# Kernel tuning notes

Hardware: AMD Instinct MI355X
Metric: run time of the kernel (lower is better)

Reference implementation:

```python
import jax, jax.numpy as jnp
import numpy as np

N = 50000; E = 800000; IN_DIM = 128; HID = 128; OUT = 128; K_TARGET = 5000


def setup_inputs() -> dict:
    key = jax.random.key(0)
    ks = jax.random.split(key, 7)
    x = jax.random.normal(ks[0], (N, IN_DIM), jnp.float32)
    edge_index = jax.random.randint(ks[1], (2, E), 0, N, dtype=jnp.int32)
    W1 = jax.random.normal(ks[2], (IN_DIM, HID), jnp.float32) / np.float32(np.sqrt(IN_DIM))
    b1 = jnp.zeros((HID,), jnp.float32)
    W2 = jax.random.normal(ks[3], (HID, OUT), jnp.float32) / np.float32(np.sqrt(HID))
    b2 = jnp.zeros((OUT,), jnp.float32)
    w_score = jax.random.normal(ks[4], (HID,), jnp.float32) / np.float32(np.sqrt(HID))
    W_skip = jax.random.normal(ks[5], (HID, OUT), jnp.float32) / np.float32(np.sqrt(HID))
    b_skip = jnp.zeros((OUT,), jnp.float32)
    return dict(x=x, edge_index=edge_index, W1=W1, b1=b1, W2=W2, b2=b2,
                w_score=w_score, W_skip=W_skip, b_skip=b_skip)


def _gcn(h_in, row, col, W, b, nseg, edge_w=None):
    # PyG GCNConv with add_self_loops=True, normalize=True:
    # deg[i] = sum of incoming edge weights at col + 1 (self loop, weight 1)
    h = h_in @ W
    w = edge_w if edge_w is not None else jnp.ones(row.shape, h.dtype)
    deg = jax.ops.segment_sum(w, col, num_segments=nseg) + 1.0
    dinv = jax.lax.rsqrt(deg)
    norm = dinv[row] * w * dinv[col]                     # [E]
    agg = jax.ops.segment_sum(norm[:, None] * h[row], col, num_segments=nseg)
    agg = agg + (dinv * dinv)[:, None] * h               # self-loop messages
    return agg + b


def _forward(x, edge_index, W1, b1, W2, b2, w_score, W_skip, b_skip):
    row, col = edge_index[0], edge_index[1]
    n = x.shape[0]
    e = row.shape[0]
    x1 = jax.nn.relu(_gcn(x, row, col, W1, b1, n))       # conv1 + relu (dropout: eval mode)
    raw = x1 @ w_score                                    # [N]
    x1g = x1 * jnp.tanh(raw)[:, None]                     # gated features
    K = min(K_TARGET, n)
    _, kept = jax.lax.top_k(raw, K)                       # sorted desc, ties -> lower index
    keep_mask = jnp.zeros((n,), bool).at[kept].set(True)
    deg = jax.ops.segment_sum(jnp.ones((e,), jnp.int32), row, num_segments=n)  # bincount(row)
    # neighbor insertion order: edge i appends col[i] to neigh[row[i]] (order 2i),
    # then row[i] to neigh[col[i]] (order 2i+1)
    owners = jnp.concatenate([row, col])
    neighs = jnp.concatenate([col, row])
    e_ar = jnp.arange(e, dtype=jnp.int32)
    order = jnp.concatenate([2 * e_ar, 2 * e_ar + 1])
    M = 2 * e + 2
    valid = keep_mask[neighs]
    comp = deg[neighs] * M + (M - 1 - order)
    comp = jnp.where(valid, comp, -1)
    best = jax.ops.segment_max(comp, owners, num_segments=n)
    has_valid = best >= 0
    is_best = valid & (comp == best[owners])              # unique per owner (order unique)
    best_neigh = jax.ops.segment_max(jnp.where(is_best, neighs, -1), owners, num_segments=n)
    cluster_of = jnp.full((n,), -1, jnp.int32).at[kept].set(jnp.arange(K, dtype=jnp.int32))
    best_global_kept = kept[jnp.argmax(deg[kept])]
    fallback = cluster_of[best_global_kept]
    assigned = jnp.where(has_valid, cluster_of[jnp.maximum(best_neigh, 0)], fallback)
    cluster_id = jnp.where(keep_mask, cluster_of, assigned)
    # mean pool per cluster (Kc == K since kept nodes carry ids 0..K-1)
    sums = jax.ops.segment_sum(x1g, cluster_id, num_segments=K)
    counts = jnp.maximum(jax.ops.segment_sum(jnp.ones((n,), x.dtype), cluster_id, num_segments=K), 1.0)
    x_p = sums / counts[:, None]
    # coarse edges: duplicates summed == unique edges weighted by counts; self-pairs dropped
    cu, cv = cluster_id[row], cluster_id[col]
    w_e = (cu != cv).astype(x.dtype)
    x_p = _gcn(x_p, cu, cv, W2, b2, K, edge_w=w_e)        # conv2 with edge_weight
    logits = x_p[cluster_id] + x1 @ W_skip + b_skip       # broadcast up + skip
    return logits


def reference(x, edge_index, W1, b1, W2, b2, w_score, W_skip, b_skip):
    logits = _forward(x, edge_index, W1, b1, W2, b2, w_score, W_skip, b_skip)
    return (logits, 0.0)
```

## Files before the change

kernel.cpp:

```cpp
#include <hip/hip_runtime.h>
#include <cstdint>

#define N_NODES 50000
#define N_EDGES 800000
#define DIM 128
#define KSEL 5000
#define MCONST (2 * N_EDGES + 2)
#define PCH 64
#define PCH2 32
#define CANDCAP 8192
#define TM 4
#define KRB ((KSEL + 255) / 256)
#define GPERS 2048

typedef unsigned long long u64;
typedef uint32_t u32;

#define FMA4(A_, S_, W_) { (A_).x = fmaf((S_), (W_).x, (A_).x); (A_).y = fmaf((S_), (W_).y, (A_).y); \
                           (A_).z = fmaf((S_), (W_).z, (A_).z); (A_).w = fmaf((S_), (W_).w, (A_).w); }

__device__ __forceinline__ void gemm_tile_body(const float4* __restrict__ W4,
                                               float xs[32][DIM], float4 acc[TM],
                                               int tx, int ty) {
#pragma unroll 8
  for (int k4 = 0; k4 < 32; k4++) {
    float4 xv[TM];
#pragma unroll
    for (int m = 0; m < TM; m++) xv[m] = *(const float4*)&xs[ty + 8 * m][k4 * 4];
#pragma unroll
    for (int j = 0; j < 4; j++) {
      float4 wv = W4[(k4 * 4 + j) * 32 + tx];
#pragma unroll
      for (int m = 0; m < TM; m++) {
        float sv = (j == 0) ? xv[m].x : (j == 1) ? xv[m].y : (j == 2) ? xv[m].z : xv[m].w;
        FMA4(acc[m], sv, wv);
      }
    }
  }
}

__global__ void gemm_tiled(const float* __restrict__ X, const float* __restrict__ W,
                           float* __restrict__ Y, int nrows) {
  __shared__ float xs[32][DIM];
  int tx = threadIdx.x & 31, ty = threadIdx.x >> 5;
  int rbase = blockIdx.x * 32;
  int nval = min(32, nrows - rbase);
  const float4* X4 = (const float4*)(X + (size_t)rbase * DIM);
  float4* xs4 = (float4*)&xs[0][0];
  for (int i = threadIdx.x; i < 32 * 32; i += 256)
    if ((i >> 5) < nval) xs4[i] = X4[i];
  __syncthreads();
  float4 acc[TM];
#pragma unroll
  for (int m = 0; m < TM; m++) acc[m] = make_float4(0.f, 0.f, 0.f, 0.f);
  gemm_tile_body((const float4*)W, xs, acc, tx, ty);
#pragma unroll
  for (int m = 0; m < TM; m++) {
    int r = rbase + ty + 8 * m;
    if (r < nrows) ((float4*)(Y + (size_t)r * DIM))[tx] = acc[m];
  }
}

__global__ void gemm_tiled_div(const float* __restrict__ S, const int* __restrict__ counts,
                               const float* __restrict__ W, float* __restrict__ Y, int nrows) {
  __shared__ float xs[32][DIM];
  int tx = threadIdx.x & 31, ty = threadIdx.x >> 5;
  int rbase = blockIdx.x * 32;
  int nval = min(32, nrows - rbase);
  const float4* X4 = (const float4*)(S + (size_t)rbase * DIM);
  float4* xs4 = (float4*)&xs[0][0];
  for (int i = threadIdx.x; i < 32 * 32; i += 256) {
    int rr = i >> 5;
    if (rr < nval) {
      float inv = 1.0f / (float)max(counts[rbase + rr], 1);
      float4 v = X4[i];
      v.x *= inv; v.y *= inv; v.z *= inv; v.w *= inv;
      xs4[i] = v;
    }
  }
  __syncthreads();
  float4 acc[TM];
#pragma unroll
  for (int m = 0; m < TM; m++) acc[m] = make_float4(0.f, 0.f, 0.f, 0.f);
  gemm_tile_body((const float4*)W, xs, acc, tx, ty);
#pragma unroll
  for (int m = 0; m < TM; m++) {
    int r = rbase + ty + 8 * m;
    if (r < nrows) ((float4*)(Y + (size_t)r * DIM))[tx] = acc[m];
  }
}

__global__ void final_tiled(const float* __restrict__ x1, const float* __restrict__ Wsk,
                            const float* __restrict__ bsk, const float* __restrict__ xp2,
                            const int* __restrict__ cluster, float* __restrict__ out) {
  __shared__ float xs[32][DIM];
  int tx = threadIdx.x & 31, ty = threadIdx.x >> 5;
  int rbase = blockIdx.x * 32;
  int nval = min(32, N_NODES - rbase);
  const float4* X4 = (const float4*)(x1 + (size_t)rbase * DIM);
  float4* xs4 = (float4*)&xs[0][0];
  for (int i = threadIdx.x; i < 32 * 32; i += 256)
    if ((i >> 5) < nval) xs4[i] = X4[i];
  __syncthreads();
  float4 acc[TM];
#pragma unroll
  for (int m = 0; m < TM; m++) acc[m] = make_float4(0.f, 0.f, 0.f, 0.f);
  gemm_tile_body((const float4*)Wsk, xs, acc, tx, ty);
  float4 bv = ((const float4*)bsk)[tx];
#pragma unroll
  for (int m = 0; m < TM; m++) {
    int r = rbase + ty + 8 * m;
    if (r < N_NODES) {
      int cl = cluster[r];
      cl = (cl < 0) ? 0 : (cl >= KSEL ? KSEL - 1 : cl);
      float4 pv = ((const float4*)(xp2 + (size_t)cl * DIM))[tx];
      float4 o;
      o.x = acc[m].x + bv.x + pv.x;
      o.y = acc[m].y + bv.y + pv.y;
      o.z = acc[m].z + bv.z + pv.z;
      o.w = acc[m].w + bv.w + pv.w;
      ((float4*)(out + (size_t)r * DIM))[tx] = o;
    }
  }
  if (blockIdx.x == 0 && threadIdx.x == 0) out[(size_t)N_NODES * DIM] = 0.0f;
}

__global__ void deg_kernel(const int* __restrict__ row, const int* __restrict__ col,
                           int* deg1, int* deg2) {
  int e = blockIdx.x * blockDim.x + threadIdx.x;
  if (e < N_EDGES) {
    atomicAdd(&deg1[col[e]], 1);
    atomicAdd(&deg2[row[e]], 1);
  }
}

__global__ void rsqrt_kernel(const int* __restrict__ deg, float* __restrict__ dinv, int n) {
  int i = blockIdx.x * blockDim.x + threadIdx.x;
  if (i < n) dinv[i] = rsqrtf((float)deg[i] + 1.0f);
}

__global__ void scan_local(const int* __restrict__ in, int* __restrict__ out,
                           int* __restrict__ bsum, int n) {
  __shared__ int s[256];
  int i = blockIdx.x * 256 + threadIdx.x;
  int v = (i < n) ? in[i] : 0;
  s[threadIdx.x] = v;
  __syncthreads();
  for (int off = 1; off < 256; off <<= 1) {
    int t = (threadIdx.x >= off) ? s[threadIdx.x - off] : 0;
    __syncthreads();
    s[threadIdx.x] += t;
    __syncthreads();
  }
  if (i < n) out[i] = s[threadIdx.x] - v;
  if (threadIdx.x == 255) bsum[blockIdx.x] = s[255];
}

__global__ void scan_bsum(int* bsum, int nb) {
  __shared__ int s[256];
  int v = (threadIdx.x < nb) ? bsum[threadIdx.x] : 0;
  s[threadIdx.x] = v;
  __syncthreads();
  for (int off = 1; off < 256; off <<= 1) {
    int t = (threadIdx.x >= off) ? s[threadIdx.x - off] : 0;
    __syncthreads();
    s[threadIdx.x] += t;
    __syncthreads();
  }
  if (threadIdx.x < nb) bsum[threadIdx.x] = s[threadIdx.x] - v;
}

__global__ void scan_add(int* out, const int* __restrict__ bsum, int n) {
  int i = blockIdx.x * 256 + threadIdx.x;
  if (i < n) out[i] += bsum[blockIdx.x];
}

__global__ void scan_small(const int* __restrict__ in, int* __restrict__ out, int n) {
  __shared__ int s[256];
  __shared__ int carry;
  if (threadIdx.x == 0) carry = 0;
  __syncthreads();
  for (int base = 0; base < n; base += 256) {
    int i = base + threadIdx.x;
    int v = (i < n) ? in[i] : 0;
    s[threadIdx.x] = v;
    __syncthreads();
    for (int off = 1; off < 256; off <<= 1) {
      int t = (threadIdx.x >= off) ? s[threadIdx.x - off] : 0;
      __syncthreads();
      s[threadIdx.x] += t;
      __syncthreads();
    }
    int c = carry;
    if (i < n) out[i] = c + s[threadIdx.x] - v;
    __syncthreads();
    if (threadIdx.x == 255) carry = c + s[255];
    __syncthreads();
  }
  if (threadIdx.x == 0) out[n] = carry;
}

__global__ void fill_ecsr(const int* __restrict__ row, const int* __restrict__ col,
                          const int* __restrict__ start, int* cursor, int* payload) {
  int e = blockIdx.x * blockDim.x + threadIdx.x;
  if (e < N_EDGES) {
    int c = col[e];
    int p = start[c] + atomicAdd(&cursor[c], 1);
    if (p >= 0 && p < N_EDGES) payload[p] = row[e];
  }
}

__global__ void fill_members(const int* __restrict__ cluster, const int* __restrict__ startn,
                             int* cursorn, int* members) {
  int i = blockIdx.x * blockDim.x + threadIdx.x;
  if (i < N_NODES) {
    int c = cluster[i];
    int p = startn[c] + atomicAdd(&cursorn[c], 1);
    if (p >= 0 && p < N_NODES) members[p] = i;
  }
}

__global__ void gcn1_gather(const int* __restrict__ srcs, const int* __restrict__ start,
                            const int* __restrict__ deg1, const float* __restrict__ dinv,
                            const float* __restrict__ h, const float* __restrict__ b1,
                            const float* __restrict__ wscore,
                            float* __restrict__ B, float* __restrict__ gate,
                            u64* __restrict__ key) {
  int lane = threadIdx.x & 63;
  int g = lane >> 5, l32 = lane & 31;
  int wid = blockIdx.x * (blockDim.x >> 6) + (threadIdx.x >> 6);
  int nw = gridDim.x * (blockDim.x >> 6);
  const float4* h4 = (const float4*)h;
  float4 wsv = ((const float4*)wscore)[l32];
  float4 b1v = ((const float4*)b1)[l32];
  int v = wid;
  int s0 = 0, n = 0; float di = 0.f;
  if (v < N_NODES) { s0 = start[v]; n = deg1[v]; di = dinv[v]; }
  while (v < N_NODES) {
    int vn = v + nw;
    int s0n = 0, nn = 0; float din = 0.f;
    if (vn < N_NODES) { s0n = start[vn]; nn = deg1[vn]; din = dinv[vn]; }
    float4 hself = h4[(size_t)v * 32 + l32];
    float4 acc0 = make_float4(0.f, 0.f, 0.f, 0.f);
    float4 acc1 = make_float4(0.f, 0.f, 0.f, 0.f);
    int k = g;
    int ra0 = (k < n) ? srcs[s0 + k] : -1;
    int ra1 = (k + 2 < n) ? srcs[s0 + k + 2] : -1;
    while (ra0 >= 0) {
      int rb0 = (k + 4 < n) ? srcs[s0 + k + 4] : -1;
      int rb1 = (k + 6 < n) ? srcs[s0 + k + 6] : -1;
      float w0 = dinv[ra0];
      float4 hv0 = h4[(size_t)ra0 * 32 + l32];
      if (ra1 >= 0) {
        float w1 = dinv[ra1];
        float4 hv1 = h4[(size_t)ra1 * 32 + l32];
        FMA4(acc0, w0, hv0);
        FMA4(acc1, w1, hv1);
      } else {
        FMA4(acc0, w0, hv0);
      }
      ra0 = rb0; ra1 = rb1; k += 4;
    }
    acc0.x += acc1.x; acc0.y += acc1.y; acc0.z += acc1.z; acc0.w += acc1.w;
    acc0.x += __shfl_xor(acc0.x, 32);
    acc0.y += __shfl_xor(acc0.y, 32);
    acc0.z += __shfl_xor(acc0.z, 32);
    acc0.w += __shfl_xor(acc0.w, 32);
    float dd = di * di;
    float4 vv;
    vv.x = acc0.x * di + dd * hself.x + b1v.x;
    vv.y = acc0.y * di + dd * hself.y + b1v.y;
    vv.z = acc0.z * di + dd * hself.z + b1v.z;
    vv.w = acc0.w * di + dd * hself.w + b1v.w;
    vv.x = vv.x > 0.f ? vv.x : 0.f;
    vv.y = vv.y > 0.f ? vv.y : 0.f;
    vv.z = vv.z > 0.f ? vv.z : 0.f;
    vv.w = vv.w > 0.f ? vv.w : 0.f;
    if (lane < 32) ((float4*)(B + (size_t)v * DIM))[l32] = vv;
    float sd = vv.x * wsv.x + vv.y * wsv.y + vv.z * wsv.z + vv.w * wsv.w;
    sd += __shfl_xor(sd, 1);
    sd += __shfl_xor(sd, 2);
    sd += __shfl_xor(sd, 4);
    sd += __shfl_xor(sd, 8);
    sd += __shfl_xor(sd, 16);
    if (lane == 0) {
      gate[v] = tanhf(sd);
      u32 b = __float_as_uint(sd);
      if ((b << 1) == 0u) b = 0u;
      u32 ord = (b & 0x80000000u) ? ~b : (b | 0x80000000u);
      key[v] = (((u64)(~ord)) << 32) | (u32)v;
    }
    v = vn; s0 = s0n; n = nn; di = din;
  }
}

__global__ void hist1_kernel(const u64* __restrict__ key, int* __restrict__ hist) {
  int i = blockIdx.x * blockDim.x + threadIdx.x;
  if (i < N_NODES) atomicAdd(&hist[(int)(key[i] >> 52)], 1);
}

__global__ void hist2_kernel(const u64* __restrict__ key, const int* __restrict__ selb,
                             int* __restrict__ hist) {
  int i = blockIdx.x * blockDim.x + threadIdx.x;
  if (i < N_NODES) {
    u64 k = key[i];
    if ((int)(k >> 52) == selb[0]) atomicAdd(&hist[(int)((k >> 40) & 0xFFF)], 1);
  }
}

__global__ void pick_kernel(const int* __restrict__ hist, int K_imm, int* __restrict__ selb,
                            int rem_in_slot, int bin_out_slot, int rem_out_slot) {
  __shared__ int s[256];
  int t = threadIdx.x;
  int base = t * 16;
  int loc[16];
  int sum = 0;
#pragma unroll
  for (int k = 0; k < 16; k++) { loc[k] = hist[base + k]; sum += loc[k]; }
  s[t] = sum;
  __syncthreads();
  for (int off = 1; off < 256; off <<= 1) {
    int v = (t >= off) ? s[t - off] : 0;
    __syncthreads();
    s[t] += v;
    __syncthreads();
  }
  int target = (K_imm >= 0) ? K_imm : selb[rem_in_slot];
  int prev = (t == 0) ? 0 : s[t - 1];
  if (prev < target && target <= s[t]) {
    int cum = prev;
#pragma unroll
    for (int k = 0; k < 16; k++) {
      cum += loc[k];
      if (cum >= target) {
        selb[bin_out_slot] = base + k;
        selb[rem_out_slot] = target - (cum - loc[k]);
        break;
      }
    }
  }
}

__global__ void collect_kernel(const u64* __restrict__ key, const int* __restrict__ selb,
                               u64* __restrict__ cand, int* __restrict__ ccnt) {
  int i = blockIdx.x * blockDim.x + threadIdx.x;
  if (i < N_NODES) {
    u64 k = key[i];
    if ((int)(k >> 52) == selb[0] && (int)((k >> 40) & 0xFFF) == selb[2]) {
      int p = atomicAdd(ccnt, 1);
      if (p < CANDCAP) cand[p] = k;
    }
  }
}

__global__ void thresh_kernel(const u64* __restrict__ cand, const int* __restrict__ ccnt,
                              const int* __restrict__ selb, u64* __restrict__ T) {
  int c = min(*ccnt, CANDCAP);
  int R = selb[3];
  for (int p = threadIdx.x; p < c; p += 256) {
    u64 kp = cand[p];
    int cnt = 0;
    for (int q = 0; q < c; q++) cnt += (cand[q] < kp) ? 1 : 0;
    if (cnt == R - 1) *T = kp;
  }
}

__global__ void compact_kernel(const u64* __restrict__ key, const u64* __restrict__ T,
                               int* __restrict__ krank, u64* __restrict__ kkey,
                               int* __restrict__ kidx, int* __restrict__ kcnt) {
  int i = blockIdx.x * blockDim.x + threadIdx.x;
  if (i < N_NODES) {
    krank[i] = -1;
    u64 k = key[i];
    if (k <= *T) {
      int p = atomicAdd(kcnt, 1);
      if (p < KSEL + 16) {
        kkey[p] = k;
        kidx[p] = i;
      }
    }
  }
}

__global__ void krank_count(const u64* __restrict__ kkey, int* __restrict__ rankc) {
  int p = blockIdx.x * 256 + threadIdx.x;
  u64 mykey = (p < KSEL) ? kkey[p] : ~0ull;
  int qbase = blockIdx.y * 256;
  __shared__ u64 sk[256];
  int j = qbase + threadIdx.x;
  sk[threadIdx.x] = (j < KSEL) ? kkey[j] : ~0ull;
  __syncthreads();
  int lim = min(256, KSEL - qbase);
  int cnt = 0;
#pragma unroll 8
  for (int q = 0; q < lim; q++) cnt += (sk[q] < mykey) ? 1 : 0;
  if (p < KSEL && cnt) atomicAdd(&rankc[p], cnt);
}

__global__ void krank_final(const int* __restrict__ rankc, const int* __restrict__ kidx,
                            const int* __restrict__ deg2, int* __restrict__ krank,
                            u64* fbkey) {
  int p = blockIdx.x * 256 + threadIdx.x;
  if (p < KSEL) {
    int node = kidx[p];
    if (node >= 0 && node < N_NODES) {
      int cnt = rankc[p];
      krank[node] = cnt;
      u64 fk = (((u64)(deg2[node] + 1)) << 32) | (u32)(KSEL - 1 - cnt);
      atomicMax(fbkey, fk);
    }
  }
}

__global__ void bestneigh_kernel(const int* __restrict__ row, const int* __restrict__ col,
                                 const int* __restrict__ krank, const int* __restrict__ deg2,
                                 u64* __restrict__ best) {
  int e = blockIdx.x * blockDim.x + threadIdx.x;
  if (e < N_EDGES) {
    int r = row[e], c = col[e];
    if (krank[c] >= 0) {
      u64 comp = (u64)deg2[c] * (u64)MCONST + (u64)(MCONST - 1 - 2 * e);
      atomicMax(&best[r], comp + 1);
    }
    if (krank[r] >= 0) {
      u64 comp = (u64)deg2[r] * (u64)MCONST + (u64)(MCONST - 2 - 2 * e);
      atomicMax(&best[c], comp + 1);
    }
  }
}

__global__ void assign_kernel(const int* __restrict__ krank, const u64* __restrict__ best,
                              const int* __restrict__ row, const int* __restrict__ col,
                              const u64* __restrict__ fbkey,
                              int* __restrict__ cluster, int* __restrict__ counts) {
  int i = blockIdx.x * blockDim.x + threadIdx.x;
  if (i >= N_NODES) return;
  int c;
  int rk = krank[i];
  if (rk >= 0) {
    c = rk;
  } else {
    u64 b = best[i];
    if (b > 0) {
      u64 comp = b - 1;
      int rem = (int)(comp % (u64)MCONST);
      int ord = MCONST - 1 - rem;
      int e = ord >> 1;
      int nb = (ord & 1) ? row[e] : col[e];
      c = krank[nb];
    } else {
      c = KSEL - 1 - (int)((*fbkey) & 0xffffffffu);
    }
  }
  c = (c < 0) ? 0 : (c >= KSEL ? KSEL - 1 : c);
  cluster[i] = c;
  atomicAdd(&counts[c], 1);
}

__global__ void pool_chunk(const int* __restrict__ members, const int* __restrict__ startn,
                           const float* __restrict__ x1, const float* __restrict__ gate,
                           float* __restrict__ sums) {
  int cb = blockIdx.x * PCH;
  if (cb >= N_NODES) return;
  int ce = min(cb + PCH, N_NODES);
  __shared__ int pl[PCH];
  for (int k = threadIdx.x; k < ce - cb; k += DIM) pl[k] = members[cb + k];
  __syncthreads();
  int lo = 0, hi = KSEL - 1;
  while (lo < hi) { int mid = (lo + hi + 1) >> 1; if (startn[mid] <= cb) lo = mid; else hi = mid - 1; }
  int c = lo;
  int segend = startn[c + 1];
  int t = threadIdx.x;
  float acc = 0.f;
  for (int k = cb; k < ce; k++) {
    int j = pl[k - cb];
    acc = fmaf(gate[j], x1[j * DIM + t], acc);
    int k1 = k + 1;
    if (k1 == segend || k1 == ce) {
      atomicAdd(&sums[c * DIM + t], acc);
      acc = 0.f;
      if (k1 == segend && k1 < ce) {
        while (c < KSEL - 1 && startn[c + 1] <= k1) c++;
        segend = startn[c + 1];
      }
    }
  }
}

__global__ void map_csrc(const int* __restrict__ payload, const int* __restrict__ cluster,
                         int* __restrict__ csrc) {
  int p = blockIdx.x * blockDim.x + threadIdx.x;
  if (p < N_EDGES) csrc[p] = cluster[payload[p]];
}

__global__ void cdeg_kernel(const int* __restrict__ csrc, const int* __restrict__ start,
                            const int* __restrict__ deg1, const int* __restrict__ cluster,
                            int* __restrict__ degc) {
  int v = blockIdx.x * blockDim.x + threadIdx.x;
  if (v >= N_NODES) return;
  int cv = cluster[v];
  int s0 = start[v], n = deg1[v], cnt = 0;
  for (int k = 0; k < n; k++) cnt += (csrc[s0 + k] != cv) ? 1 : 0;
  if (cnt) atomicAdd(&degc[cv], cnt);
}

__global__ void coarse_chunk(const int* __restrict__ members, const int* __restrict__ startn,
                             const int* __restrict__ start, const int* __restrict__ deg1,
                             const int* __restrict__ csrc, const float* __restrict__ dinvc,
                             const float* __restrict__ h2, float* __restrict__ agg2) {
  int cb = blockIdx.x * PCH2;
  if (cb >= N_NODES) return;
  int ce = min(cb + PCH2, N_NODES);
  int t = threadIdx.x;
  int g = t >> 5, l32 = t & 31;
  __shared__ int pm[PCH2];
  __shared__ float red4[4][DIM];
  __shared__ int sinter[4];
  for (int k = t; k < ce - cb; k += 128) pm[k] = members[cb + k];
  __syncthreads();
  int lo = 0, hi = KSEL - 1;
  while (lo < hi) { int mid = (lo + hi + 1) >> 1; if (startn[mid] <= cb) lo = mid; else hi = mid - 1; }
  int c = lo;
  int segend = startn[c + 1];
  const float4* h24 = (const float4*)h2;
  float4 acc = make_float4(0.f, 0.f, 0.f, 0.f);
  int inter = 0;
  int m = cb;
  int v0 = pm[0];
  int s0 = start[v0], n = deg1[v0];
  while (m < ce) {
    int m1 = m + 1;
    int s0n = 0, nn = 0;
    if (m1 < ce) { int v1 = pm[m1 - cb]; s0n = start[v1]; nn = deg1[v1]; }
    int k = g;
    int ca0 = (k < n) ? csrc[s0 + k] : -1;
    int ca1 = (k + 4 < n) ? csrc[s0 + k + 4] : -1;
    while (ca0 >= 0) {
      int cb0 = (k + 8 < n) ? csrc[s0 + k + 8] : -1;
      int cb1 = (k + 12 < n) ? csrc[s0 + k + 12] : -1;
      float w0 = (ca0 == c) ? 0.f : dinvc[ca0];
      inter += (ca0 != c) ? 1 : 0;
      float4 hv0 = h24[(size_t)ca0 * 32 + l32];
      if (ca1 >= 0) {
        float w1 = (ca1 == c) ? 0.f : dinvc[ca1];
        inter += (ca1 != c) ? 1 : 0;
        float4 hv1 = h24[(size_t)ca1 * 32 + l32];
        FMA4(acc, w0, hv0);
        FMA4(acc, w1, hv1);
      } else {
        FMA4(acc, w0, hv0);
      }
      ca0 = cb0; ca1 = cb1; k += 8;
    }
    if (m1 == segend || m1 == ce) {
      *(float4*)&red4[g][l32 * 4] = acc;
      if (l32 == 0) sinter[g] = inter;
      __syncthreads();
      if (sinter[0] + sinter[1] + sinter[2] + sinter[3] > 0) {
        float sv = red4[0][t] + red4[1][t] + red4[2][t] + red4[3][t];
        atomicAdd(&agg2[(size_t)c * DIM + t], sv);
      }
      __syncthreads();
      acc = make_float4(0.f, 0.f, 0.f, 0.f);
      inter = 0;
      if (m1 == segend && m1 < ce) {
        while (c < KSEL - 1 && startn[c + 1] <= m1) c++;
        segend = startn[c + 1];
      }
    }
    m = m1; s0 = s0n; n = nn;
  }
}

__global__ void combine2(const float* __restrict__ agg2, const float* __restrict__ h2,
                         const float* __restrict__ dinvc, const float* __restrict__ b2,
                         float* __restrict__ xp2) {
  int gid = blockIdx.x * blockDim.x + threadIdx.x;
  int c = gid >> 7, d = gid & 127;
  if (c < KSEL) {
    float dc = dinvc[c];
    xp2[gid] = agg2[gid] * dc + dc * dc * h2[gid] + b2[d];
  }
}

extern "C" void kernel_launch(void* const* d_in, const int* in_sizes, int n_in,
                              void* d_out, int out_size, void* d_ws, size_t ws_size,
                              hipStream_t stream) {
  const float* x      = (const float*)d_in[0];
  const int*   eidx   = (const int*)d_in[1];
  const float* W1     = (const float*)d_in[2];
  const float* b1     = (const float*)d_in[3];
  const float* W2     = (const float*)d_in[4];
  const float* b2     = (const float*)d_in[5];
  const float* wscore = (const float*)d_in[6];
  const float* Wsk    = (const float*)d_in[7];
  const float* bsk    = (const float*)d_in[8];
  float* out = (float*)d_out;

  const int* row = eidx;
  const int* col = eidx + N_EDGES;

  char* ws = (char*)d_ws;
#define ALIGN16(v) (((v) + 15) & ~(size_t)15)
  size_t off = 0;
#define CARVE(ptr_t, name, bytes) ptr_t name = (ptr_t)(ws + off); off = ALIGN16(off + (bytes))
  size_t h_off = off;
  CARVE(float*, h, (size_t)N_NODES * DIM * 4);
  CARVE(float*, B, (size_t)N_NODES * DIM * 4);
  CARVE(int*, payload, (size_t)N_EDGES * 4);
  CARVE(u64*, key, (size_t)N_NODES * 8);
  CARVE(float*, gate, (size_t)N_NODES * 4);
  CARVE(float*, dinv, (size_t)N_NODES * 4);
  CARVE(int*, start, (size_t)N_NODES * 4);
  CARVE(int*, bsum, 256 * 4);
  size_t zA = off;
  CARVE(int*, deg1, (size_t)N_NODES * 4);
  CARVE(int*, deg2, (size_t)N_NODES * 4);
  CARVE(int*, cursor, (size_t)N_NODES * 4);
  size_t zAsize = off - zA;

  size_t ho = h_off;
#define CARVE2(ptr_t, name, bytes) ptr_t name = (ptr_t)(ws + ho); ho = ALIGN16(ho + (bytes))
  CARVE2(int*, cluster, (size_t)N_NODES * 4);
  CARVE2(int*, members, (size_t)N_NODES * 4);
  CARVE2(int*, startn, (size_t)(KSEL + 1) * 4);
  CARVE2(float*, dinvc, (size_t)KSEL * 4);
  CARVE2(float*, h2, (size_t)KSEL * DIM * 4);
  CARVE2(int*, csrc, (size_t)N_EDGES * 4);
  size_t zB = ho;
  CARVE2(u64*, best, (size_t)N_NODES * 8);
  CARVE2(int*, counts, (size_t)KSEL * 4);
  CARVE2(int*, degc, (size_t)KSEL * 4);
  CARVE2(int*, cursorn, (size_t)KSEL * 4);
  CARVE2(float*, sums, (size_t)KSEL * DIM * 4);
  CARVE2(float*, agg2, (size_t)KSEL * DIM * 4);
  CARVE2(u64*, fbkey, 8);
  CARVE2(int*, hist1, 4096 * 4);
  CARVE2(int*, hist2, 4096 * 4);
  CARVE2(int*, rankc, (size_t)KSEL * 4);
  CARVE2(int*, ccnt, 16);
  CARVE2(int*, kcnt, 16);
  size_t zBsize = ho - zB;
  CARVE2(int*, krank, (size_t)N_NODES * 4);
  CARVE2(u64*, cand, (size_t)CANDCAP * 8);
  CARVE2(u64*, kkey, (size_t)(KSEL + 16) * 8);
  CARVE2(int*, kidx, (size_t)(KSEL + 16) * 4);
  CARVE2(int*, selb, 4 * 4);
  CARVE2(u64*, Tkey, 8);
  float* xp2 = sums;
  (void)ws_size; (void)out_size; (void)n_in; (void)in_sizes;

  const int eb  = (N_EDGES + 255) / 256;
  const int nb  = (N_NODES + 255) / 256;
  const int kbs = (KSEL + 255) / 256;
  const int pcb = (N_NODES + PCH - 1) / PCH;
  const int ccb = (N_NODES + PCH2 - 1) / PCH2;
  const int gtb = (N_NODES + 31) / 32;
  const int gkb = (KSEL + 31) / 32;

  hipMemsetAsync(ws + zA, 0, zAsize, stream);

  gemm_tiled<<<gtb, 256, 0, stream>>>(x, W1, h, N_NODES);
  deg_kernel<<<eb, 256, 0, stream>>>(row, col, deg1, deg2);
  rsqrt_kernel<<<nb, 256, 0, stream>>>(deg1, dinv, N_NODES);
  scan_local<<<nb, 256, 0, stream>>>(deg1, start, bsum, N_NODES);
  scan_bsum<<<1, 256, 0, stream>>>(bsum, nb);
  scan_add<<<nb, 256, 0, stream>>>(start, bsum, N_NODES);
  fill_ecsr<<<eb, 256, 0, stream>>>(row, col, start, cursor, payload);
  gcn1_gather<<<GPERS, 256, 0, stream>>>(payload, start, deg1, dinv, h, b1, wscore,
                                         B, gate, key);
  hipMemsetAsync(ws + zB, 0, zBsize, stream);

  hist1_kernel<<<nb, 256, 0, stream>>>(key, hist1);
  pick_kernel<<<1, 256, 0, stream>>>(hist1, KSEL, selb, 0, 0, 1);
  hist2_kernel<<<nb, 256, 0, stream>>>(key, selb, hist2);
  pick_kernel<<<1, 256, 0, stream>>>(hist2, -1, selb, 1, 2, 3);
  collect_kernel<<<nb, 256, 0, stream>>>(key, selb, cand, ccnt);
  thresh_kernel<<<1, 256, 0, stream>>>(cand, ccnt, selb, Tkey);
  compact_kernel<<<nb, 256, 0, stream>>>(key, Tkey, krank, kkey, kidx, kcnt);
  krank_count<<<dim3(KRB, KRB), 256, 0, stream>>>(kkey, rankc);
  krank_final<<<kbs, 256, 0, stream>>>(rankc, kidx, deg2, krank, fbkey);

  bestneigh_kernel<<<eb, 256, 0, stream>>>(row, col, krank, deg2, best);
  assign_kernel<<<nb, 256, 0, stream>>>(krank, best, row, col, fbkey, cluster, counts);

  scan_small<<<1, 256, 0, stream>>>(counts, startn, KSEL);
  fill_members<<<nb, 256, 0, stream>>>(cluster, startn, cursorn, members);
  pool_chunk<<<pcb, DIM, 0, stream>>>(members, startn, B, gate, sums);
  map_csrc<<<eb, 256, 0, stream>>>(payload, cluster, csrc);
  cdeg_kernel<<<nb, 256, 0, stream>>>(csrc, start, deg1, cluster, degc);
  rsqrt_kernel<<<kbs, 256, 0, stream>>>(degc, dinvc, KSEL);

  gemm_tiled_div<<<gkb, 256, 0, stream>>>(sums, counts, W2, h2, KSEL);
  coarse_chunk<<<ccb, 128, 0, stream>>>(members, startn, start, deg1, csrc, dinvc,
                                        h2, agg2);
  combine2<<<(KSEL * DIM) / 256, 256, 0, stream>>>(agg2, h2, dinvc, b2, xp2);

  final_tiled<<<gtb, 256, 0, stream>>>(B, Wsk, bsk, xp2, cluster, out);
}
```

Baseline: 697.0 us.

## Batch-load neighbor indices and weights per wave, broadcast via shuffles in gathers

```diff
diff --git a/kernel.cpp b/kernel.cpp
--- a/kernel.cpp
+++ b/kernel.cpp
@@ -7,7 +7,7 @@
 #define KSEL 5000
 #define MCONST (2 * N_EDGES + 2)
 #define PCH 64
-#define PCH2 32
+#define PCH2 16
 #define CANDCAP 8192
 #define TM 4
 #define KRB ((KSEL + 255) / 256)
@@ -228,38 +228,50 @@
                             u64* __restrict__ key) {
   int lane = threadIdx.x & 63;
   int g = lane >> 5, l32 = lane & 31;
+  int gbase = g << 5;
   int wid = blockIdx.x * (blockDim.x >> 6) + (threadIdx.x >> 6);
   int nw = gridDim.x * (blockDim.x >> 6);
   const float4* h4 = (const float4*)h;
   float4 wsv = ((const float4*)wscore)[l32];
   float4 b1v = ((const float4*)b1)[l32];
-  int v = wid;
-  int s0 = 0, n = 0; float di = 0.f;
-  if (v < N_NODES) { s0 = start[v]; n = deg1[v]; di = dinv[v]; }
-  while (v < N_NODES) {
-    int vn = v + nw;
-    int s0n = 0, nn = 0; float din = 0.f;
-    if (vn < N_NODES) { s0n = start[vn]; nn = deg1[vn]; din = dinv[vn]; }
+  for (int v = wid; v < N_NODES; v += nw) {
+    int s0 = start[v], n = deg1[v];
+    float di = dinv[v];
     float4 hself = h4[(size_t)v * 32 + l32];
     float4 acc0 = make_float4(0.f, 0.f, 0.f, 0.f);
     float4 acc1 = make_float4(0.f, 0.f, 0.f, 0.f);
-    int k = g;
-    int ra0 = (k < n) ? srcs[s0 + k] : -1;
-    int ra1 = (k + 2 < n) ? srcs[s0 + k + 2] : -1;
-    while (ra0 >= 0) {
-      int rb0 = (k + 4 < n) ? srcs[s0 + k + 4] : -1;
-      int rb1 = (k + 6 < n) ? srcs[s0 + k + 6] : -1;
-      float w0 = dinv[ra0];
-      float4 hv0 = h4[(size_t)ra0 * 32 + l32];
-      if (ra1 >= 0) {
-        float w1 = dinv[ra1];
-        float4 hv1 = h4[(size_t)ra1 * 32 + l32];
-        FMA4(acc0, w0, hv0);
-        FMA4(acc1, w1, hv1);
-      } else {
-        FMA4(acc0, w0, hv0);
-      }
-      ra0 = rb0; ra1 = rb1; k += 4;
+    for (int base = 0; base < n; base += 64) {
+      int mm = min(64, n - base);
+      int idx = base + (l32 << 1) + g;
+      int csv = (idx < n) ? srcs[s0 + idx] : 0;
+      float wvl = (idx < n) ? dinv[csv] : 0.f;
+      int cnt = (mm + 1 - g) >> 1;
+      int i = 0;
+      for (; i + 3 < cnt; i += 4) {
+        int r0 = __shfl(csv, gbase + i),     r1 = __shfl(csv, gbase + i + 1);
+        int r2 = __shfl(csv, gbase + i + 2), r3 = __shfl(csv, gbase + i + 3);
+        float w0 = __shfl(wvl, gbase + i),     w1 = __shfl(wvl, gbase + i + 1);
+        float w2 = __shfl(wvl, gbase + i + 2), w3 = __shfl(wvl, gbase + i + 3);
+        float4 a0 = h4[(size_t)r0 * 32 + l32];
+        float4 a1 = h4[(size_t)r1 * 32 + l32];
+        float4 a2 = h4[(size_t)r2 * 32 + l32];
+        float4 a3 = h4[(size_t)r3 * 32 + l32];
+        FMA4(acc0, w0, a0); FMA4(acc1, w1, a1);
+        FMA4(acc0, w2, a2); FMA4(acc1, w3, a3);
+      }
+      for (; i + 1 < cnt; i += 2) {
+        int r0 = __shfl(csv, gbase + i), r1 = __shfl(csv, gbase + i + 1);
+        float w0 = __shfl(wvl, gbase + i), w1 = __shfl(wvl, gbase + i + 1);
+        float4 a0 = h4[(size_t)r0 * 32 + l32];
+        float4 a1 = h4[(size_t)r1 * 32 + l32];
+        FMA4(acc0, w0, a0); FMA4(acc1, w1, a1);
+      }
+      if (i < cnt) {
+        int r0 = __shfl(csv, gbase + i);
+        float w0 = __shfl(wvl, gbase + i);
+        float4 a0 = h4[(size_t)r0 * 32 + l32];
+        FMA4(acc0, w0, a0);
+      }
     }
     acc0.x += acc1.x; acc0.y += acc1.y; acc0.z += acc1.z; acc0.w += acc1.w;
     acc0.x += __shfl_xor(acc0.x, 32);
@@ -290,7 +302,6 @@
       u32 ord = (b & 0x80000000u) ? ~b : (b | 0x80000000u);
       key[v] = (((u64)(~ord)) << 32) | (u32)v;
     }
-    v = vn; s0 = s0n; n = nn; di = din;
   }
 }
 
@@ -458,6 +469,7 @@
 }
 
 __global__ void pool_chunk(const int* __restrict__ members, const int* __restrict__ startn,
+                           const int* __restrict__ cluster,
                            const float* __restrict__ x1, const float* __restrict__ gate,
                            float* __restrict__ sums) {
   int cb = blockIdx.x * PCH;
@@ -466,9 +478,7 @@
   __shared__ int pl[PCH];
   for (int k = threadIdx.x; k < ce - cb; k += DIM) pl[k] = members[cb + k];
   __syncthreads();
-  int lo = 0, hi = KSEL - 1;
-  while (lo < hi) { int mid = (lo + hi + 1) >> 1; if (startn[mid] <= cb) lo = mid; else hi = mid - 1; }
-  int c = lo;
+  int c = cluster[pl[0]];
   int segend = startn[c + 1];
   int t = threadIdx.x;
   float acc = 0.f;
@@ -505,6 +515,7 @@
 }
 
 __global__ void coarse_chunk(const int* __restrict__ members, const int* __restrict__ startn,
+                             const int* __restrict__ cluster,
                              const int* __restrict__ start, const int* __restrict__ deg1,
                              const int* __restrict__ csrc, const float* __restrict__ dinvc,
                              const float* __restrict__ h2, float* __restrict__ agg2) {
@@ -513,18 +524,15 @@
   int ce = min(cb + PCH2, N_NODES);
   int t = threadIdx.x;
   int g = t >> 5, l32 = t & 31;
+  int gbase = (g & 1) << 5;
   __shared__ int pm[PCH2];
   __shared__ float red4[4][DIM];
-  __shared__ int sinter[4];
   for (int k = t; k < ce - cb; k += 128) pm[k] = members[cb + k];
   __syncthreads();
-  int lo = 0, hi = KSEL - 1;
-  while (lo < hi) { int mid = (lo + hi + 1) >> 1; if (startn[mid] <= cb) lo = mid; else hi = mid - 1; }
-  int c = lo;
+  int c = cluster[pm[0]];
   int segend = startn[c + 1];
   const float4* h24 = (const float4*)h2;
   float4 acc = make_float4(0.f, 0.f, 0.f, 0.f);
-  int inter = 0;
   int m = cb;
   int v0 = pm[0];
   int s0 = start[v0], n = deg1[v0];
@@ -532,37 +540,39 @@
     int m1 = m + 1;
     int s0n = 0, nn = 0;
     if (m1 < ce) { int v1 = pm[m1 - cb]; s0n = start[v1]; nn = deg1[v1]; }
-    int k = g;
-    int ca0 = (k < n) ? csrc[s0 + k] : -1;
-    int ca1 = (k + 4 < n) ? csrc[s0 + k + 4] : -1;
-    while (ca0 >= 0) {
-      int cb0 = (k + 8 < n) ? csrc[s0 + k + 8] : -1;
-      int cb1 = (k + 12 < n) ? csrc[s0 + k + 12] : -1;
-      float w0 = (ca0 == c) ? 0.f : dinvc[ca0];
-      inter += (ca0 != c) ? 1 : 0;
-      float4 hv0 = h24[(size_t)ca0 * 32 + l32];
-      if (ca1 >= 0) {
-        float w1 = (ca1 == c) ? 0.f : dinvc[ca1];
-        inter += (ca1 != c) ? 1 : 0;
-        float4 hv1 = h24[(size_t)ca1 * 32 + l32];
-        FMA4(acc, w0, hv0);
-        FMA4(acc, w1, hv1);
-      } else {
-        FMA4(acc, w0, hv0);
-      }
-      ca0 = cb0; ca1 = cb1; k += 8;
+    for (int base = 0; base < n; base += 128) {
+      int mm = min(128, n - base);
+      int idx = base + (l32 << 2) + g;
+      int csv = (idx < n) ? csrc[s0 + idx] : 0;
+      float wvl = (idx < n && csv != c) ? dinvc[csv] : 0.f;
+      int cnt = (mm + 3 - g) >> 2;
+      int i = 0;
+      for (; i + 3 < cnt; i += 4) {
+        int r0 = __shfl(csv, gbase + i),     r1 = __shfl(csv, gbase + i + 1);
+        int r2 = __shfl(csv, gbase + i + 2), r3 = __shfl(csv, gbase + i + 3);
+        float w0 = __shfl(wvl, gbase + i),     w1 = __shfl(wvl, gbase + i + 1);
+        float w2 = __shfl(wvl, gbase + i + 2), w3 = __shfl(wvl, gbase + i + 3);
+        float4 a0 = h24[(size_t)r0 * 32 + l32];
+        float4 a1 = h24[(size_t)r1 * 32 + l32];
+        float4 a2 = h24[(size_t)r2 * 32 + l32];
+        float4 a3 = h24[(size_t)r3 * 32 + l32];
+        FMA4(acc, w0, a0); FMA4(acc, w1, a1);
+        FMA4(acc, w2, a2); FMA4(acc, w3, a3);
+      }
+      for (; i < cnt; i++) {
+        int r0 = __shfl(csv, gbase + i);
+        float w0 = __shfl(wvl, gbase + i);
+        float4 a0 = h24[(size_t)r0 * 32 + l32];
+        FMA4(acc, w0, a0);
+      }
     }
     if (m1 == segend || m1 == ce) {
       *(float4*)&red4[g][l32 * 4] = acc;
-      if (l32 == 0) sinter[g] = inter;
       __syncthreads();
-      if (sinter[0] + sinter[1] + sinter[2] + sinter[3] > 0) {
-        float sv = red4[0][t] + red4[1][t] + red4[2][t] + red4[3][t];
-        atomicAdd(&agg2[(size_t)c * DIM + t], sv);
-      }
+      float sv = red4[0][t] + red4[1][t] + red4[2][t] + red4[3][t];
+      atomicAdd(&agg2[(size_t)c * DIM + t], sv);
       __syncthreads();
       acc = make_float4(0.f, 0.f, 0.f, 0.f);
-      inter = 0;
       if (m1 == segend && m1 < ce) {
         while (c < KSEL - 1 && startn[c + 1] <= m1) c++;
         segend = startn[c + 1];
@@ -686,14 +696,14 @@
 
   scan_small<<<1, 256, 0, stream>>>(counts, startn, KSEL);
   fill_members<<<nb, 256, 0, stream>>>(cluster, startn, cursorn, members);
-  pool_chunk<<<pcb, DIM, 0, stream>>>(members, startn, B, gate, sums);
+  pool_chunk<<<pcb, DIM, 0, stream>>>(members, startn, cluster, B, gate, sums);
   map_csrc<<<eb, 256, 0, stream>>>(payload, cluster, csrc);
   cdeg_kernel<<<nb, 256, 0, stream>>>(csrc, start, deg1, cluster, degc);
   rsqrt_kernel<<<kbs, 256, 0, stream>>>(degc, dinvc, KSEL);
 
   gemm_tiled_div<<<gkb, 256, 0, stream>>>(sums, counts, W2, h2, KSEL);
-  coarse_chunk<<<ccb, 128, 0, stream>>>(members, startn, start, deg1, csrc, dinvc,
-                                        h2, agg2);
+  coarse_chunk<<<ccb, 128, 0, stream>>>(members, startn, cluster, start, deg1, csrc,
+                                        dinvc, h2, agg2);
   combine2<<<(KSEL * DIM) / 256, 256, 0, stream>>>(agg2, h2, dinvc, b2, xp2);
 
   final_tiled<<<gtb, 256, 0, stream>>>(B, Wsk, bsk, xp2, cluster, out);
```

Result: faster. 662.4 us (-5.0%).
